# Kernel tuning notes

Measured on AMD Instinct MI355X. Metric: run time of the kernel, lower is better.

Reference implementation:

```python
import jax, jax.numpy as jnp
import numpy as np

EMBED_DIM = 512
NUM_HEADS = 8
DEPTH = EMBED_DIM // NUM_HEADS
B, S = 2, 4096


def setup_inputs() -> dict:
    key = jax.random.key(0)
    ks = jax.random.split(key, 11)
    s = 1.0 / np.sqrt(EMBED_DIM)
    return {
        "q": jax.random.normal(ks[0], (B, S, EMBED_DIM), jnp.float32),
        "k": jax.random.normal(ks[1], (B, S, EMBED_DIM), jnp.float32),
        "v": jax.random.normal(ks[2], (B, S, EMBED_DIM), jnp.float32),
        "mask": jnp.zeros((B, 1, 1, S), jnp.float32),  # additive mask: 1=masked, 0=keep
        "Wq": jax.random.normal(ks[3], (EMBED_DIM, EMBED_DIM), jnp.float32) * s,
        "bq": jnp.zeros((EMBED_DIM,), jnp.float32),
        "Wk": jax.random.normal(ks[4], (EMBED_DIM, EMBED_DIM), jnp.float32) * s,
        "bk": jnp.zeros((EMBED_DIM,), jnp.float32),
        "Wv": jax.random.normal(ks[5], (EMBED_DIM, EMBED_DIM), jnp.float32) * s,
        "bv": jnp.zeros((EMBED_DIM,), jnp.float32),
        "Wo": jax.random.normal(ks[6], (EMBED_DIM, EMBED_DIM), jnp.float32) * s,
        "bo": jnp.zeros((EMBED_DIM,), jnp.float32),
    }


def _split_heads(x):
    b, s, _ = x.shape
    return x.reshape(b, s, NUM_HEADS, DEPTH).transpose(0, 2, 1, 3)  # [B,H,S,D]


def reference(q, k, v, mask, Wq, bq, Wk, bk, Wv, bv, Wo, bo):
    qh = _split_heads(q @ Wq + bq)
    kh = _split_heads(k @ Wk + bk)
    vh = _split_heads(v @ Wv + bv)
    logits = jnp.einsum("bhqd,bhkd->bhqk", qh, kh) / jnp.sqrt(jnp.float32(DEPTH))
    logits = logits + mask * -1e9
    attn = jax.nn.softmax(logits, axis=-1)
    out = jnp.einsum("bhqk,bhkd->bhqd", attn, vh)
    out = out.transpose(0, 2, 1, 3).reshape(q.shape[0], -1, EMBED_DIM)
    return out @ Wo + bo
```

## Files before the change

### kernel.cpp

```cpp
#include <hip/hip_runtime.h>
#include <stdint.h>

typedef __bf16 bf16;
typedef bf16 bf16x8 __attribute__((ext_vector_type(8)));
typedef float f32x4 __attribute__((ext_vector_type(4)));
typedef float f32x16 __attribute__((ext_vector_type(16)));

#define EMBED 512
#define NHEAD 8
#define DEPTH 64
#define BATCH 2
#define SEQ 4096
#define M_TOTAL (BATCH * SEQ)

#define LOG2E 1.44269504f
#define QSCALE (0.125f * LOG2E)
#define MASKC (-1.0e9f * LOG2E)
#define DEFER_THR 10.0f

__device__ __forceinline__ void gload16(const void* g, void* l) {
  __builtin_amdgcn_global_load_lds((const __attribute__((address_space(1))) unsigned*)g,
                                   (__attribute__((address_space(3))) unsigned*)l, 16, 0, 0);
}
__device__ __forceinline__ uint32_t cvtpk(float a, float b) {
  uint32_t r;
  asm volatile("v_cvt_pk_bf16_f32 %0, %1, %2" : "=v"(r) : "v"(a), "v"(b));
  return r;
}
__device__ __forceinline__ void plswap(uint32_t& a, uint32_t& b) {
  asm volatile("v_permlane32_swap_b32 %0, %1" : "+v"(a), "+v"(b));
}
__device__ __forceinline__ float vdup(float x) {
  float r;
  asm volatile("v_mov_b32 %0, %1" : "=v"(r) : "v"(x));
  return r;
}
__device__ __forceinline__ float cross_max(float x) {
  float a = x, b = vdup(x);
  asm volatile("v_permlane32_swap_b32 %0, %1" : "+v"(a), "+v"(b));
  return fmaxf(a, b);
}
__device__ __forceinline__ float cross_sum(float x) {
  float a = x, b = vdup(x);
  asm volatile("v_permlane32_swap_b32 %0, %1" : "+v"(a), "+v"(b));
  return a + b;
}
union U4 { uint32_t u[4]; bf16x8 v; };

__global__ __launch_bounds__(256) void cvt3(const float* __restrict__ q, const float* __restrict__ k,
                                            const float* __restrict__ v, bf16* __restrict__ oq,
                                            bf16* __restrict__ ok, bf16* __restrict__ ov) {
  int z = blockIdx.y;
  const float* in = z == 0 ? q : (z == 1 ? k : v);
  bf16* out = z == 0 ? oq : (z == 1 ? ok : ov);
  size_t i = ((size_t)blockIdx.x * 256 + threadIdx.x) * 8;
  float4 f0 = *(const float4*)(in + i);
  float4 f1 = *(const float4*)(in + i + 4);
  bf16x8 o;
  o[0] = (bf16)f0.x; o[1] = (bf16)f0.y; o[2] = (bf16)f0.z; o[3] = (bf16)f0.w;
  o[4] = (bf16)f1.x; o[5] = (bf16)f1.y; o[6] = (bf16)f1.z; o[7] = (bf16)f1.w;
  *(bf16x8*)(out + i) = o;
}

__global__ __launch_bounds__(256) void transpose4(const float* __restrict__ W0, const float* __restrict__ W1,
                                                  const float* __restrict__ W2, const float* __restrict__ W3,
                                                  bf16* __restrict__ T0, bf16* __restrict__ T1,
                                                  bf16* __restrict__ T2, bf16* __restrict__ T3) {
  int z = blockIdx.z;
  const float* W = z == 0 ? W0 : (z == 1 ? W1 : (z == 2 ? W2 : W3));
  bf16* WT = z == 0 ? T0 : (z == 1 ? T1 : (z == 2 ? T2 : T3));
  __shared__ float t[32][33];
  int k0 = blockIdx.x * 32, n0 = blockIdx.y * 32;
  int x = threadIdx.x & 31, y = threadIdx.x >> 5;
#pragma unroll
  for (int yy = y; yy < 32; yy += 8)
    t[yy][x] = W[(size_t)(k0 + yy) * EMBED + n0 + x];
  __syncthreads();
#pragma unroll
  for (int yy = y; yy < 32; yy += 8)
    WT[(size_t)(n0 + yy) * EMBED + k0 + x] = (bf16)t[x][yy];
}

__device__ __forceinline__ void gemm128_body(const bf16* __restrict__ A, const bf16* __restrict__ Bt,
                                             const float* __restrict__ bias, void* __restrict__ out,
                                             float scale, int mode) {
  __shared__ __align__(16) bf16 As[128 * 64];
  __shared__ __align__(16) bf16 Bs[128 * 64];
  int tid = threadIdx.x, lane = tid & 63, w = tid >> 6;
  int g = lane >> 4, r = lane & 15;
  int n0 = blockIdx.x * 128, m0 = blockIdx.y * 128;
  int wr = (w >> 1) * 64, wc = (w & 1) * 64;

  f32x4 acc[4][4];
#pragma unroll
  for (int m = 0; m < 4; m++)
#pragma unroll
    for (int n = 0; n < 4; n++)
#pragma unroll
      for (int i = 0; i < 4; i++) acc[m][n][i] = 0.f;

  size_t aoff[4], boff[4];
#pragma unroll
  for (int i = 0; i < 4; i++) {
    int u = w * 64 + lane + i * 256;
    int row = u >> 3, scs = (u & 7) ^ (row & 7);
    aoff[i] = (size_t)(m0 + row) * EMBED + scs * 8;
    boff[i] = (size_t)(n0 + row) * EMBED + scs * 8;
  }

  for (int k0 = 0; k0 < EMBED; k0 += 64) {
#pragma unroll
    for (int i = 0; i < 4; i++) {
      gload16(A + aoff[i] + k0, &As[(w + i * 4) * 512]);
      gload16(Bt + boff[i] + k0, &Bs[(w + i * 4) * 512]);
    }
    __syncthreads();
#pragma unroll
    for (int kk = 0; kk < 64; kk += 32) {
      bf16x8 af[4], bf_[4];
#pragma unroll
      for (int m = 0; m < 4; m++) {
        int row = wr + m * 16 + r;
        af[m] = *(const bf16x8*)&As[row * 64 + (((kk >> 3) + g) ^ (r & 7)) * 8];
      }
#pragma unroll
      for (int n = 0; n < 4; n++) {
        int col = wc + n * 16 + r;
        bf_[n] = *(const bf16x8*)&Bs[col * 64 + (((kk >> 3) + g) ^ (r & 7)) * 8];
      }
      __builtin_amdgcn_s_setprio(1);
#pragma unroll
      for (int m = 0; m < 4; m++)
#pragma unroll
        for (int n = 0; n < 4; n++)
          acc[m][n] = __builtin_amdgcn_mfma_f32_16x16x32_bf16(af[m], bf_[n], acc[m][n], 0, 0, 0);
      __builtin_amdgcn_s_setprio(0);
    }
    __syncthreads();
  }

#pragma unroll
  for (int n = 0; n < 4; n++) {
    int ncol = n0 + wc + n * 16 + r;
    float bv = bias[ncol];
#pragma unroll
    for (int m = 0; m < 4; m++)
#pragma unroll
      for (int v_ = 0; v_ < 4; v_++) {
        int mrow = m0 + wr + m * 16 + g * 4 + v_;
        float val = (acc[m][n][v_] + bv) * scale;
        if (mode == 2) {
          ((float*)out)[(size_t)mrow * EMBED + ncol] = val;
        } else {
          int b = mrow >> 12, s = mrow & (SEQ - 1);
          int h = ncol >> 6, d = ncol & 63;
          size_t idx = (mode == 0) ? ((((size_t)(b * NHEAD + h)) * SEQ + s) * DEPTH + d)
                                   : ((((size_t)(b * NHEAD + h)) * DEPTH + d) * SEQ + s);
          ((bf16*)out)[idx] = (bf16)val;
        }
      }
  }
}

__global__ __launch_bounds__(256, 3) void gemm_qkv(const bf16* __restrict__ Xq, const bf16* __restrict__ Xk,
                                                   const bf16* __restrict__ Xv, const bf16* __restrict__ Tq,
                                                   const bf16* __restrict__ Tk, const bf16* __restrict__ Tv,
                                                   const float* __restrict__ bq, const float* __restrict__ bk,
                                                   const float* __restrict__ bv, bf16* __restrict__ qh,
                                                   bf16* __restrict__ kh, bf16* __restrict__ vT) {
  int z = blockIdx.z;
  const bf16* A = z == 0 ? Xq : (z == 1 ? Xk : Xv);
  const bf16* Bt = z == 0 ? Tq : (z == 1 ? Tk : Tv);
  const float* bias = z == 0 ? bq : (z == 1 ? bk : bv);
  void* out = z == 0 ? (void*)qh : (z == 1 ? (void*)kh : (void*)vT);
  float scale = z == 0 ? QSCALE : 1.0f;
  int mode = z == 2 ? 1 : 0;
  gemm128_body(A, Bt, bias, out, scale, mode);
}

__global__ __launch_bounds__(256, 3) void gemm_o(const bf16* __restrict__ A, const bf16* __restrict__ Bt,
                                                 const float* __restrict__ bias, float* __restrict__ out) {
  gemm128_body(A, Bt, bias, out, 1.0f, 2);
}

__global__ __launch_bounds__(256, 2) void flash_attn(const bf16* __restrict__ qh,
                                                     const bf16* __restrict__ kh,
                                                     const bf16* __restrict__ vT,
                                                     const float* __restrict__ mask,
                                                     bf16* __restrict__ O) {
  __shared__ __align__(16) bf16 Ks[2][4096];
  __shared__ __align__(16) bf16 Vs[2][4096];
  int tid = threadIdx.x;
  int lane = tid & 63, w = tid >> 6;
  int l31 = lane & 31, hi = lane >> 5, l7 = lane & 7;
  int bh = blockIdx.y, b = bh >> 3, h = bh & 7;
  int q0 = blockIdx.x * 128;
  const bf16* Qb = qh + (size_t)bh * SEQ * DEPTH;
  const bf16* Kb = kh + (size_t)bh * SEQ * DEPTH;
  const bf16* Vb = vT + (size_t)bh * DEPTH * SEQ;
  const float* maskb = mask + (size_t)b * SEQ;

  int srow = tid >> 3;
  int scs = (tid & 7) ^ (srow & 7);
  const bf16* kg0 = Kb + (size_t)srow * DEPTH + scs * 8;
  const bf16* vg0 = Vb + (size_t)srow * SEQ + scs * 8;
  bf16* kd0 = &Ks[0][w * 512];
  bf16* kd1 = &Ks[1][w * 512];
  bf16* vd0 = &Vs[0][w * 512];
  bf16* vd1 = &Vs[1][w * 512];

  gload16(kg0, kd0);
  gload16(kg0 + 2048, kd0 + 2048);
  gload16(vg0, vd0);
  gload16(vg0 + 32 * SEQ, vd0 + 2048);

  bf16x8 qf[4];
  {
    const bf16* qp = Qb + (size_t)(q0 + w * 32 + l31) * DEPTH + hi * 8;
#pragma unroll
    for (int s = 0; s < 4; s++) qf[s] = *(const bf16x8*)(qp + s * 16);
  }

  f32x16 oacc[2];
#pragma unroll
  for (int nb = 0; nb < 2; nb++)
#pragma unroll
    for (int i = 0; i < 16; i++) oacc[nb][i] = 0.f;
  float mrun = -__builtin_inff(), lrun = 0.f;

  __syncthreads();

  int cur = 0;
  for (int t = 0; t < SEQ / 64; ++t) {
    int kv = t * 64;
    if (t + 1 < SEQ / 64) {
      const bf16* kg = kg0 + (size_t)(kv + 64) * DEPTH;
      const bf16* vg = vg0 + (kv + 64);
      bf16* kd = cur ? kd0 : kd1;
      bf16* vd = cur ? vd0 : vd1;
      gload16(kg, kd);
      gload16(kg + 2048, kd + 2048);
      gload16(vg, vd);
      gload16(vg + 32 * SEQ, vd + 2048);
    }
    f32x4 mf[8];
#pragma unroll
    for (int m2 = 0; m2 < 2; m2++)
#pragma unroll
      for (int g = 0; g < 4; g++)
        mf[m2 * 4 + g] = *(const f32x4*)(maskb + kv + m2 * 32 + g * 8 + 4 * hi);

    const bf16* Kcur = cur ? Ks[1] : Ks[0];
    const bf16* Vcur = cur ? Vs[1] : Vs[0];

    f32x16 sacc[2];
#pragma unroll
    for (int m2 = 0; m2 < 2; m2++) {
#pragma unroll
      for (int i = 0; i < 16; i++) sacc[m2][i] = 0.f;
    }
    __builtin_amdgcn_s_setprio(1);
#pragma unroll
    for (int m2 = 0; m2 < 2; m2++)
#pragma unroll
      for (int s = 0; s < 4; s++) {
        bf16x8 kf = *(const bf16x8*)(Kcur + (m2 * 32 + l31) * 64 + (((s * 2 + hi) ^ l7) * 8));
        sacc[m2] = __builtin_amdgcn_mfma_f32_32x32x16_bf16(kf, qf[s], sacc[m2], 0, 0, 0);
      }
    __builtin_amdgcn_s_setprio(0);

#pragma unroll
    for (int m2 = 0; m2 < 2; m2++)
#pragma unroll
      for (int g = 0; g < 4; g++)
#pragma unroll
        for (int i = 0; i < 4; i++)
          sacc[m2][4 * g + i] = fmaf(mf[m2 * 4 + g][i], MASKC, sacc[m2][4 * g + i]);

    float tmx[16];
#pragma unroll
    for (int i = 0; i < 16; i++) tmx[i] = fmaxf(sacc[0][i], sacc[1][i]);
#pragma unroll
    for (int i = 0; i < 8; i++) tmx[i] = fmaxf(tmx[i], tmx[i + 8]);
#pragma unroll
    for (int i = 0; i < 4; i++) tmx[i] = fmaxf(tmx[i], tmx[i + 4]);
    float pmax = fmaxf(fmaxf(tmx[0], tmx[1]), fmaxf(tmx[2], tmx[3]));
    pmax = cross_max(pmax);

    if (__any(pmax > mrun + DEFER_THR)) {
      float mnew = fmaxf(mrun, pmax);
      float alpha = exp2f(mrun - mnew);
      lrun *= alpha;
      mrun = mnew;
#pragma unroll
      for (int r = 0; r < 16; r++) {
        float af = __shfl(alpha, (r & 3) + 8 * (r >> 2) + 4 * hi);
        oacc[0][r] *= af;
        oacc[1][r] *= af;
      }
    }

    float p[32];
    float rsv[4] = {0.f, 0.f, 0.f, 0.f};
#pragma unroll
    for (int m2 = 0; m2 < 2; m2++)
#pragma unroll
      for (int i = 0; i < 16; i++) {
        float pv = __builtin_amdgcn_exp2f(sacc[m2][i] - mrun);
        p[m2 * 16 + i] = pv;
        rsv[i & 3] += pv;
      }
    float rsum = (rsv[0] + rsv[1]) + (rsv[2] + rsv[3]);
    lrun += cross_sum(rsum);

    bf16x8 pa[4];
#pragma unroll
    for (int m2 = 0; m2 < 2; m2++) {
      uint32_t c0 = cvtpk(p[m2 * 16 + 0], p[m2 * 16 + 1]);
      uint32_t c1 = cvtpk(p[m2 * 16 + 2], p[m2 * 16 + 3]);
      uint32_t d0 = cvtpk(p[m2 * 16 + 4], p[m2 * 16 + 5]);
      uint32_t d1 = cvtpk(p[m2 * 16 + 6], p[m2 * 16 + 7]);
      plswap(c0, d0);
      plswap(c1, d1);
      U4 e; e.u[0] = c0; e.u[1] = c1; e.u[2] = d0; e.u[3] = d1;
      pa[m2 * 2 + 0] = e.v;
      uint32_t c2 = cvtpk(p[m2 * 16 + 8], p[m2 * 16 + 9]);
      uint32_t c3 = cvtpk(p[m2 * 16 + 10], p[m2 * 16 + 11]);
      uint32_t d2 = cvtpk(p[m2 * 16 + 12], p[m2 * 16 + 13]);
      uint32_t d3 = cvtpk(p[m2 * 16 + 14], p[m2 * 16 + 15]);
      plswap(c2, d2);
      plswap(c3, d3);
      U4 o; o.u[0] = c2; o.u[1] = c3; o.u[2] = d2; o.u[3] = d3;
      pa[m2 * 2 + 1] = o.v;
    }

    __builtin_amdgcn_s_setprio(1);
#pragma unroll
    for (int nb = 0; nb < 2; nb++)
#pragma unroll
      for (int ks = 0; ks < 4; ks++) {
        bf16x8 vf = *(const bf16x8*)(Vcur + (nb * 32 + l31) * 64 + (((ks * 2 + hi) ^ l7) * 8));
        oacc[nb] = __builtin_amdgcn_mfma_f32_32x32x16_bf16(pa[ks], vf, oacc[nb], 0, 0, 0);
      }
    __builtin_amdgcn_s_setprio(0);

    __syncthreads();
    cur ^= 1;
  }

  float invl = 1.0f / lrun;
  bf16* Ob = O + ((size_t)(b * SEQ + q0 + w * 32)) * EMBED + h * DEPTH + l31;
#pragma unroll
  for (int r = 0; r < 16; r++) {
    int cr = (r & 3) + 8 * (r >> 2) + 4 * hi;
    float iv = __shfl(invl, cr);
    Ob[(size_t)cr * EMBED + 0] = (bf16)(oacc[0][r] * iv);
    Ob[(size_t)cr * EMBED + 32] = (bf16)(oacc[1][r] * iv);
  }
}

extern "C" void kernel_launch(void* const* d_in, const int* in_sizes, int n_in,
                              void* d_out, int out_size, void* d_ws, size_t ws_size,
                              hipStream_t stream) {
  (void)in_sizes; (void)n_in; (void)out_size; (void)ws_size;
  const float* q = (const float*)d_in[0];
  const float* k = (const float*)d_in[1];
  const float* v = (const float*)d_in[2];
  const float* mask = (const float*)d_in[3];
  const float* Wq = (const float*)d_in[4];
  const float* bq = (const float*)d_in[5];
  const float* Wk = (const float*)d_in[6];
  const float* bk = (const float*)d_in[7];
  const float* Wv = (const float*)d_in[8];
  const float* bv = (const float*)d_in[9];
  const float* Wo = (const float*)d_in[10];
  const float* bo = (const float*)d_in[11];

  const size_t NX = (size_t)M_TOTAL * EMBED;
  const size_t NW = (size_t)EMBED * EMBED;
  bf16* Xq = (bf16*)d_ws;
  bf16* Xk = Xq + NX;
  bf16* Xv = Xk + NX;
  bf16* WTq = Xv + NX;
  bf16* WTk = WTq + NW;
  bf16* WTv = WTk + NW;
  bf16* WTo = WTv + NW;
  bf16* qh = WTo + NW;
  bf16* kh = qh + NX;
  bf16* vT = kh + NX;
  bf16* Ow = vT + NX;

  cvt3<<<dim3(NX / 2048, 3), 256, 0, stream>>>(q, k, v, Xq, Xk, Xv);
  transpose4<<<dim3(16, 16, 4), 256, 0, stream>>>(Wq, Wk, Wv, Wo, WTq, WTk, WTv, WTo);

  gemm_qkv<<<dim3(EMBED / 128, M_TOTAL / 128, 3), 256, 0, stream>>>(
      Xq, Xk, Xv, WTq, WTk, WTv, bq, bk, bv, qh, kh, vT);

  flash_attn<<<dim3(SEQ / 128, BATCH * NHEAD), 256, 0, stream>>>(qh, kh, vT, mask, Ow);

  gemm_o<<<dim3(EMBED / 128, M_TOTAL / 128), 256, 0, stream>>>(Ow, WTo, bo, (float*)d_out);
}
```

Measured before the change: 255.6 us.

## Split KV across warp halves with 64-row Q tiles per warp in flash attention

Flash attention now launches 512-thread blocks over 256 queries. Each group of four warps handles half of the KV sequence, and each warp processes 64 query rows, so K fragments loaded from LDS are reused across two Q sub-tiles. The two KV-half partial results are merged through shared memory at the end using the running max and sum. This halves the grid to 256 blocks, which may underfill the CUs, and adds register pressure and a merge step. The GEMM launch bounds are also lowered from 3 to 2 blocks per CU.

```diff
diff --git a/kernel.cpp b/kernel.cpp
--- a/kernel.cpp
+++ b/kernel.cpp
@@ -12,6 +12,8 @@
 #define BATCH 2
 #define SEQ 4096
 #define M_TOTAL (BATCH * SEQ)
+#define KVH 2048
+#define NT (KVH / 64)
 
 #define LOG2E 1.44269504f
 #define QSCALE (0.125f * LOG2E)
@@ -162,7 +164,7 @@
   }
 }
 
-__global__ __launch_bounds__(256, 3) void gemm_qkv(const bf16* __restrict__ Xq, const bf16* __restrict__ Xk,
+__global__ __launch_bounds__(256, 2) void gemm_qkv(const bf16* __restrict__ Xq, const bf16* __restrict__ Xk,
                                                    const bf16* __restrict__ Xv, const bf16* __restrict__ Tq,
                                                    const bf16* __restrict__ Tk, const bf16* __restrict__ Tv,
                                                    const float* __restrict__ bq, const float* __restrict__ bk,
@@ -178,160 +180,169 @@
   gemm128_body(A, Bt, bias, out, scale, mode);
 }
 
-__global__ __launch_bounds__(256, 3) void gemm_o(const bf16* __restrict__ A, const bf16* __restrict__ Bt,
+__global__ __launch_bounds__(256, 2) void gemm_o(const bf16* __restrict__ A, const bf16* __restrict__ Bt,
                                                  const float* __restrict__ bias, float* __restrict__ out) {
   gemm128_body(A, Bt, bias, out, 1.0f, 2);
 }
 
-__global__ __launch_bounds__(256, 2) void flash_attn(const bf16* __restrict__ qh,
+__global__ __launch_bounds__(512, 2) void flash_attn(const bf16* __restrict__ qh,
                                                      const bf16* __restrict__ kh,
                                                      const bf16* __restrict__ vT,
                                                      const float* __restrict__ mask,
                                                      bf16* __restrict__ O) {
-  __shared__ __align__(16) bf16 Ks[2][4096];
-  __shared__ __align__(16) bf16 Vs[2][4096];
+  __shared__ __align__(16) unsigned char smem[65536];
+  __shared__ float Sm[4][64];
+  __shared__ float Sl[4][64];
+  bf16* KV = (bf16*)smem;
+
   int tid = threadIdx.x;
   int lane = tid & 63, w = tid >> 6;
   int l31 = lane & 31, hi = lane >> 5, l7 = lane & 7;
+  int qs = w & 3, half = w >> 2;
   int bh = blockIdx.y, b = bh >> 3, h = bh & 7;
-  int q0 = blockIdx.x * 128;
+  int q0 = blockIdx.x * 256;
   const bf16* Qb = qh + (size_t)bh * SEQ * DEPTH;
   const bf16* Kb = kh + (size_t)bh * SEQ * DEPTH;
   const bf16* Vb = vT + (size_t)bh * DEPTH * SEQ;
-  const float* maskb = mask + (size_t)b * SEQ;
+  const float* maskb = mask + (size_t)b * SEQ + half * KVH;
 
   int srow = tid >> 3;
   int scs = (tid & 7) ^ (srow & 7);
   const bf16* kg0 = Kb + (size_t)srow * DEPTH + scs * 8;
   const bf16* vg0 = Vb + (size_t)srow * SEQ + scs * 8;
-  bf16* kd0 = &Ks[0][w * 512];
-  bf16* kd1 = &Ks[1][w * 512];
-  bf16* vd0 = &Vs[0][w * 512];
-  bf16* vd1 = &Vs[1][w * 512];
-
-  gload16(kg0, kd0);
-  gload16(kg0 + 2048, kd0 + 2048);
-  gload16(vg0, vd0);
-  gload16(vg0 + 32 * SEQ, vd0 + 2048);
-
-  bf16x8 qf[4];
-  {
-    const bf16* qp = Qb + (size_t)(q0 + w * 32 + l31) * DEPTH + hi * 8;
-#pragma unroll
-    for (int s = 0; s < 4; s++) qf[s] = *(const bf16x8*)(qp + s * 16);
-  }
-
-  f32x16 oacc[2];
-#pragma unroll
-  for (int nb = 0; nb < 2; nb++)
-#pragma unroll
-    for (int i = 0; i < 16; i++) oacc[nb][i] = 0.f;
-  float mrun = -__builtin_inff(), lrun = 0.f;
+  int wofs = w * 512;
+
+#define STAGE(buf, kv)                                                              \
+  do {                                                                              \
+    gload16(kg0 + (size_t)(kv)*DEPTH, KV + (buf)*16384 + wofs);                     \
+    gload16(kg0 + (size_t)((kv) + KVH) * DEPTH, KV + (buf)*16384 + 4096 + wofs);    \
+    gload16(vg0 + (kv), KV + (buf)*16384 + 8192 + wofs);                            \
+    gload16(vg0 + ((kv) + KVH), KV + (buf)*16384 + 12288 + wofs);                   \
+  } while (0)
+
+  STAGE(0, 0);
+
+  bf16x8 qf[2][4];
+#pragma unroll
+  for (int q2 = 0; q2 < 2; q2++) {
+    const bf16* qp = Qb + (size_t)(q0 + qs * 64 + q2 * 32 + l31) * DEPTH + hi * 8;
+#pragma unroll
+    for (int s = 0; s < 4; s++) qf[q2][s] = *(const bf16x8*)(qp + s * 16);
+  }
+
+  f32x16 oacc[2][2];
+#pragma unroll
+  for (int q2 = 0; q2 < 2; q2++)
+#pragma unroll
+    for (int nb = 0; nb < 2; nb++)
+#pragma unroll
+      for (int i = 0; i < 16; i++) oacc[q2][nb][i] = 0.f;
+  float mrun[2] = {-__builtin_inff(), -__builtin_inff()};
+  float lrun[2] = {0.f, 0.f};
 
   __syncthreads();
 
   int cur = 0;
-  for (int t = 0; t < SEQ / 64; ++t) {
+  for (int t = 0; t < NT; ++t) {
     int kv = t * 64;
-    if (t + 1 < SEQ / 64) {
-      const bf16* kg = kg0 + (size_t)(kv + 64) * DEPTH;
-      const bf16* vg = vg0 + (kv + 64);
-      bf16* kd = cur ? kd0 : kd1;
-      bf16* vd = cur ? vd0 : vd1;
-      gload16(kg, kd);
-      gload16(kg + 2048, kd + 2048);
-      gload16(vg, vd);
-      gload16(vg + 32 * SEQ, vd + 2048);
-    }
-    f32x4 mf[8];
+    if (t + 1 < NT) STAGE(cur ^ 1, kv + 64);
+
+    const bf16* Kcur = KV + cur * 16384 + half * 4096;
+    const bf16* Vcur = KV + cur * 16384 + 8192 + half * 4096;
+
+    f32x4 mf[2][4];
 #pragma unroll
     for (int m2 = 0; m2 < 2; m2++)
 #pragma unroll
       for (int g = 0; g < 4; g++)
-        mf[m2 * 4 + g] = *(const f32x4*)(maskb + kv + m2 * 32 + g * 8 + 4 * hi);
-
-    const bf16* Kcur = cur ? Ks[1] : Ks[0];
-    const bf16* Vcur = cur ? Vs[1] : Vs[0];
-
-    f32x16 sacc[2];
-#pragma unroll
-    for (int m2 = 0; m2 < 2; m2++) {
-#pragma unroll
-      for (int i = 0; i < 16; i++) sacc[m2][i] = 0.f;
-    }
-    __builtin_amdgcn_s_setprio(1);
+        mf[m2][g] = *(const f32x4*)(maskb + kv + m2 * 32 + g * 8 + 4 * hi);
+
+    bf16x8 kf[2][4];
 #pragma unroll
     for (int m2 = 0; m2 < 2; m2++)
 #pragma unroll
-      for (int s = 0; s < 4; s++) {
-        bf16x8 kf = *(const bf16x8*)(Kcur + (m2 * 32 + l31) * 64 + (((s * 2 + hi) ^ l7) * 8));
-        sacc[m2] = __builtin_amdgcn_mfma_f32_32x32x16_bf16(kf, qf[s], sacc[m2], 0, 0, 0);
-      }
-    __builtin_amdgcn_s_setprio(0);
-
-#pragma unroll
-    for (int m2 = 0; m2 < 2; m2++)
-#pragma unroll
-      for (int g = 0; g < 4; g++)
-#pragma unroll
-        for (int i = 0; i < 4; i++)
-          sacc[m2][4 * g + i] = fmaf(mf[m2 * 4 + g][i], MASKC, sacc[m2][4 * g + i]);
-
-    float tmx[16];
-#pragma unroll
-    for (int i = 0; i < 16; i++) tmx[i] = fmaxf(sacc[0][i], sacc[1][i]);
-#pragma unroll
-    for (int i = 0; i < 8; i++) tmx[i] = fmaxf(tmx[i], tmx[i + 8]);
-#pragma unroll
-    for (int i = 0; i < 4; i++) tmx[i] = fmaxf(tmx[i], tmx[i + 4]);
-    float pmax = fmaxf(fmaxf(tmx[0], tmx[1]), fmaxf(tmx[2], tmx[3]));
-    pmax = cross_max(pmax);
-
-    if (__any(pmax > mrun + DEFER_THR)) {
-      float mnew = fmaxf(mrun, pmax);
-      float alpha = exp2f(mrun - mnew);
-      lrun *= alpha;
-      mrun = mnew;
-#pragma unroll
-      for (int r = 0; r < 16; r++) {
-        float af = __shfl(alpha, (r & 3) + 8 * (r >> 2) + 4 * hi);
-        oacc[0][r] *= af;
-        oacc[1][r] *= af;
-      }
-    }
-
-    float p[32];
-    float rsv[4] = {0.f, 0.f, 0.f, 0.f};
-#pragma unroll
-    for (int m2 = 0; m2 < 2; m2++)
-#pragma unroll
-      for (int i = 0; i < 16; i++) {
-        float pv = __builtin_amdgcn_exp2f(sacc[m2][i] - mrun);
-        p[m2 * 16 + i] = pv;
-        rsv[i & 3] += pv;
-      }
-    float rsum = (rsv[0] + rsv[1]) + (rsv[2] + rsv[3]);
-    lrun += cross_sum(rsum);
-
-    bf16x8 pa[4];
-#pragma unroll
-    for (int m2 = 0; m2 < 2; m2++) {
-      uint32_t c0 = cvtpk(p[m2 * 16 + 0], p[m2 * 16 + 1]);
-      uint32_t c1 = cvtpk(p[m2 * 16 + 2], p[m2 * 16 + 3]);
-      uint32_t d0 = cvtpk(p[m2 * 16 + 4], p[m2 * 16 + 5]);
-      uint32_t d1 = cvtpk(p[m2 * 16 + 6], p[m2 * 16 + 7]);
-      plswap(c0, d0);
-      plswap(c1, d1);
-      U4 e; e.u[0] = c0; e.u[1] = c1; e.u[2] = d0; e.u[3] = d1;
-      pa[m2 * 2 + 0] = e.v;
-      uint32_t c2 = cvtpk(p[m2 * 16 + 8], p[m2 * 16 + 9]);
-      uint32_t c3 = cvtpk(p[m2 * 16 + 10], p[m2 * 16 + 11]);
-      uint32_t d2 = cvtpk(p[m2 * 16 + 12], p[m2 * 16 + 13]);
-      uint32_t d3 = cvtpk(p[m2 * 16 + 14], p[m2 * 16 + 15]);
-      plswap(c2, d2);
-      plswap(c3, d3);
-      U4 o; o.u[0] = c2; o.u[1] = c3; o.u[2] = d2; o.u[3] = d3;
-      pa[m2 * 2 + 1] = o.v;
+      for (int s = 0; s < 4; s++)
+        kf[m2][s] = *(const bf16x8*)(Kcur + (m2 * 32 + l31) * 64 + (((s * 2 + hi) ^ l7) * 8));
+
+    bf16x8 pa[2][4];
+#pragma unroll
+    for (int q2 = 0; q2 < 2; q2++) {
+      f32x16 sacc[2];
+#pragma unroll
+      for (int m2 = 0; m2 < 2; m2++)
+#pragma unroll
+        for (int i = 0; i < 16; i++) sacc[m2][i] = 0.f;
+      __builtin_amdgcn_s_setprio(1);
+#pragma unroll
+      for (int m2 = 0; m2 < 2; m2++)
+#pragma unroll
+        for (int s = 0; s < 4; s++)
+          sacc[m2] = __builtin_amdgcn_mfma_f32_32x32x16_bf16(kf[m2][s], qf[q2][s], sacc[m2], 0, 0, 0);
+      __builtin_amdgcn_s_setprio(0);
+
+#pragma unroll
+      for (int m2 = 0; m2 < 2; m2++)
+#pragma unroll
+        for (int g = 0; g < 4; g++)
+#pragma unroll
+          for (int i = 0; i < 4; i++)
+            sacc[m2][4 * g + i] = fmaf(mf[m2][g][i], MASKC, sacc[m2][4 * g + i]);
+
+      float tmx[16];
+#pragma unroll
+      for (int i = 0; i < 16; i++) tmx[i] = fmaxf(sacc[0][i], sacc[1][i]);
+#pragma unroll
+      for (int i = 0; i < 8; i++) tmx[i] = fmaxf(tmx[i], tmx[i + 8]);
+#pragma unroll
+      for (int i = 0; i < 4; i++) tmx[i] = fmaxf(tmx[i], tmx[i + 4]);
+      float pmax = fmaxf(fmaxf(tmx[0], tmx[1]), fmaxf(tmx[2], tmx[3]));
+      pmax = cross_max(pmax);
+
+      if (__any(pmax > mrun[q2] + DEFER_THR)) {
+        float mnew = fmaxf(mrun[q2], pmax);
+        float alpha = exp2f(mrun[q2] - mnew);
+        lrun[q2] *= alpha;
+        mrun[q2] = mnew;
+#pragma unroll
+        for (int r = 0; r < 16; r++) {
+          float af = __shfl(alpha, (r & 3) + 8 * (r >> 2) + 4 * hi);
+          oacc[q2][0][r] *= af;
+          oacc[q2][1][r] *= af;
+        }
+      }
+
+      float p[32];
+      float rsv[4] = {0.f, 0.f, 0.f, 0.f};
+#pragma unroll
+      for (int m2 = 0; m2 < 2; m2++)
+#pragma unroll
+        for (int i = 0; i < 16; i++) {
+          float pv = __builtin_amdgcn_exp2f(sacc[m2][i] - mrun[q2]);
+          p[m2 * 16 + i] = pv;
+          rsv[i & 3] += pv;
+        }
+      float rsum = (rsv[0] + rsv[1]) + (rsv[2] + rsv[3]);
+      lrun[q2] += cross_sum(rsum);
+
+#pragma unroll
+      for (int m2 = 0; m2 < 2; m2++) {
+        uint32_t c0 = cvtpk(p[m2 * 16 + 0], p[m2 * 16 + 1]);
+        uint32_t c1 = cvtpk(p[m2 * 16 + 2], p[m2 * 16 + 3]);
+        uint32_t d0 = cvtpk(p[m2 * 16 + 4], p[m2 * 16 + 5]);
+        uint32_t d1 = cvtpk(p[m2 * 16 + 6], p[m2 * 16 + 7]);
+        plswap(c0, d0);
+        plswap(c1, d1);
+        U4 e; e.u[0] = c0; e.u[1] = c1; e.u[2] = d0; e.u[3] = d1;
+        pa[q2][m2 * 2 + 0] = e.v;
+        uint32_t c2 = cvtpk(p[m2 * 16 + 8], p[m2 * 16 + 9]);
+        uint32_t c3 = cvtpk(p[m2 * 16 + 10], p[m2 * 16 + 11]);
+        uint32_t d2 = cvtpk(p[m2 * 16 + 12], p[m2 * 16 + 13]);
+        uint32_t d3 = cvtpk(p[m2 * 16 + 14], p[m2 * 16 + 15]);
+        plswap(c2, d2);
+        plswap(c3, d3);
+        U4 o; o.u[0] = c2; o.u[1] = c3; o.u[2] = d2; o.u[3] = d3;
+        pa[q2][m2 * 2 + 1] = o.v;
+      }
     }
 
     __builtin_amdgcn_s_setprio(1);
@@ -340,7 +351,8 @@
 #pragma unroll
       for (int ks = 0; ks < 4; ks++) {
         bf16x8 vf = *(const bf16x8*)(Vcur + (nb * 32 + l31) * 64 + (((ks * 2 + hi) ^ l7) * 8));
-        oacc[nb] = __builtin_amdgcn_mfma_f32_32x32x16_bf16(pa[ks], vf, oacc[nb], 0, 0, 0);
+        oacc[0][nb] = __builtin_amdgcn_mfma_f32_32x32x16_bf16(pa[0][ks], vf, oacc[0][nb], 0, 0, 0);
+        oacc[1][nb] = __builtin_amdgcn_mfma_f32_32x32x16_bf16(pa[1][ks], vf, oacc[1][nb], 0, 0, 0);
       }
     __builtin_amdgcn_s_setprio(0);
 
@@ -348,15 +360,56 @@
     cur ^= 1;
   }
 
-  float invl = 1.0f / lrun;
-  bf16* Ob = O + ((size_t)(b * SEQ + q0 + w * 32)) * EMBED + h * DEPTH + l31;
-#pragma unroll
-  for (int r = 0; r < 16; r++) {
-    int cr = (r & 3) + 8 * (r >> 2) + 4 * hi;
-    float iv = __shfl(invl, cr);
-    Ob[(size_t)cr * EMBED + 0] = (bf16)(oacc[0][r] * iv);
-    Ob[(size_t)cr * EMBED + 32] = (bf16)(oacc[1][r] * iv);
-  }
+  float* Oex = (float*)smem;
+  if (half == 1) {
+    if (hi == 0) {
+#pragma unroll
+      for (int q2 = 0; q2 < 2; q2++) {
+        Sm[qs][q2 * 32 + l31] = mrun[q2];
+        Sl[qs][q2 * 32 + l31] = lrun[q2];
+      }
+    }
+    float* Op = Oex + qs * 4096;
+#pragma unroll
+    for (int q2 = 0; q2 < 2; q2++)
+#pragma unroll
+      for (int nb = 0; nb < 2; nb++)
+#pragma unroll
+        for (int r = 0; r < 16; r++) {
+          int cr = (r & 3) + 8 * (r >> 2) + 4 * hi;
+          Op[(q2 * 32 + cr) * 64 + nb * 32 + l31] = oacc[q2][nb][r];
+        }
+  }
+  __syncthreads();
+  if (half == 0) {
+    float s0[2], s1[2];
+#pragma unroll
+    for (int q2 = 0; q2 < 2; q2++) {
+      float m1 = Sm[qs][q2 * 32 + l31];
+      float l1 = Sl[qs][q2 * 32 + l31];
+      float mm = fmaxf(mrun[q2], m1);
+      float e0 = exp2f(mrun[q2] - mm);
+      float e1 = exp2f(m1 - mm);
+      float inv = 1.0f / (lrun[q2] * e0 + l1 * e1);
+      s0[q2] = e0 * inv;
+      s1[q2] = e1 * inv;
+    }
+    float* Op = Oex + qs * 4096;
+    bf16* Ob = O + ((size_t)(b * SEQ + q0 + qs * 64)) * EMBED + h * DEPTH + l31;
+#pragma unroll
+    for (int q2 = 0; q2 < 2; q2++)
+#pragma unroll
+      for (int nb = 0; nb < 2; nb++)
+#pragma unroll
+        for (int r = 0; r < 16; r++) {
+          int cr = (r & 3) + 8 * (r >> 2) + 4 * hi;
+          float a0 = __shfl(s0[q2], cr);
+          float a1 = __shfl(s1[q2], cr);
+          float o1 = Op[(q2 * 32 + cr) * 64 + nb * 32 + l31];
+          Ob[(size_t)(q2 * 32 + cr) * EMBED + nb * 32] = (bf16)(oacc[q2][nb][r] * a0 + o1 * a1);
+        }
+  }
+#undef STAGE
 }
 
 extern "C" void kernel_launch(void* const* d_in, const int* in_sizes, int n_in,
@@ -396,7 +449,7 @@
   gemm_qkv<<<dim3(EMBED / 128, M_TOTAL / 128, 3), 256, 0, stream>>>(
       Xq, Xk, Xv, WTq, WTk, WTv, bq, bk, bv, qh, kh, vT);
 
-  flash_attn<<<dim3(SEQ / 128, BATCH * NHEAD), 256, 0, stream>>>(qh, kh, vT, mask, Ow);
+  flash_attn<<<dim3(SEQ / 256, BATCH * NHEAD), 512, 0, stream>>>(qh, kh, vT, mask, Ow);
 
   gemm_o<<<dim3(EMBED / 128, M_TOTAL / 128), 256, 0, stream>>>(Ow, WTo, bo, (float*)d_out);
 }
```

Result: no change. 251.9 us (-1.4%).
